# Performance work log

Hardware: AMD Instinct MI355X
Metric: run time of the kernel (lower is better)

The kernel has to match this reference:

```python
import jax, jax.numpy as jnp
import numpy as np

FILTERS = 128
KERNEL = 3
N_TAPS = KERNEL * KERNEL  # 9
STRIDES = 1


def setup_inputs() -> dict:
    key = jax.random.key(0)
    k1, k2, k3 = jax.random.split(key, 3)
    x = jax.random.normal(k1, (8, 128, 128, 64), dtype=jnp.float32)
    offsets = jax.random.normal(k2, (8, 128, 128, 2 * N_TAPS), dtype=jnp.float32)
    W = jax.random.normal(k3, (64, N_TAPS, FILTERS), dtype=jnp.float32) * 0.05
    return {"x": x, "offsets": offsets, "W": W}


def _blin(x, offsets, strides):
    # x: (m, Hi, Wi, C); offsets: (m, Ho, Wo, 2N) -> sampled (m, Ho, Wo, N, C)
    m, Hi, Wi, C = x.shape
    _, Ho, Wo, twoN = offsets.shape
    N = twoN // 2
    off = offsets.reshape(m, Ho, Wo, N, 2)
    base_i = jnp.arange(0, Hi, strides, dtype=jnp.float32)[:Ho]  # strided input rows
    base_j = jnp.arange(0, Wi, strides, dtype=jnp.float32)[:Wo]
    ci = jnp.clip(base_i[None, :, None, None] + off[..., 0], 0.0, Hi - 1.0)  # (m,Ho,Wo,N)
    cj = jnp.clip(base_j[None, None, :, None] + off[..., 1], 0.0, Wi - 1.0)
    i0 = jnp.floor(ci).astype(jnp.int32)
    i1 = jnp.ceil(ci).astype(jnp.int32)
    j0 = jnp.floor(cj).astype(jnp.int32)
    j1 = jnp.ceil(cj).astype(jnp.int32)
    fi = (ci - i0.astype(jnp.float32))[..., None]  # (m,Ho,Wo,N,1)
    fj = (cj - j0.astype(jnp.float32))[..., None]
    b = jnp.arange(m)[:, None, None, None]
    # four-corner gathers over channel vectors -> (m,Ho,Wo,N,C)
    v_lt = x[b, i0, j0]
    v_rt = x[b, i0, j1]
    v_lb = x[b, i1, j0]
    v_rb = x[b, i1, j1]
    v_t = v_lt + (v_rt - v_lt) * fj
    v_b = v_lb + (v_rb - v_lb) * fj
    return v_t + (v_b - v_t) * fi


def reference(x, offsets, W):
    sampled = _blin(x, offsets, STRIDES)  # (m,Ho,Wo,N,C)
    # sum over kernel taps N and channels C with W (C,N,filters)
    return jnp.einsum('mhwnc,cnf->mhwf', sampled, W)
```

## Files before the change

kernel.cpp:

```cpp
#include <hip/hip_runtime.h>
#include <hip/hip_fp16.h>
#include <cstddef>


typedef __attribute__((ext_vector_type(8))) _Float16 f16x8;
typedef __attribute__((ext_vector_type(4))) float    f32x4;

struct __align__(16) H2x4 { __half2 a, b, c, d; };


__global__ void cvt_x_kernel(const float* __restrict__ x, __half* __restrict__ xh) {
    int i = blockIdx.x * 256 + threadIdx.x;
    const float4* p = (const float4*)x + (size_t)i * 2;
    float4 a = p[0], b = p[1];
    H2x4 o;
    o.a = __floats2half2_rn(a.x, a.y);
    o.b = __floats2half2_rn(a.z, a.w);
    o.c = __floats2half2_rn(b.x, b.y);
    o.d = __floats2half2_rn(b.z, b.w);
    ((H2x4*)xh)[i] = o;
}

__global__ void cvt_w_kernel(const float* __restrict__ W, __half* __restrict__ wt2) {
    int idx = blockIdx.x * 256 + threadIdx.x;
    if (idx >= 9 * 4 * 4 * 64 * 8) return;
    int e  = idx & 7;
    int ln = (idx >> 3) & 63;
    int fr = (idx >> 9) & 3;
    int wv = (idx >> 11) & 3;
    int n  = idx >> 13;
    int nf = fr >> 1, kf = fr & 1;
    int r = ln & 15, g = ln >> 4;
    int c = kf * 32 + g * 8 + e;
    int f = wv * 32 + nf * 16 + r;
    wt2[idx] = __float2half_rn(W[((size_t)c * 9 + n) * 128 + f]);
}



struct Gather {
    H2x4 v00, v01, v10, v11;
    __half2 wA, wB;
};

__device__ inline void issue_gather(const char* __restrict__ ximg,
                                    const unsigned short* __restrict__ pb,
                                    const __half2 (*__restrict__ pw)[2],
                                    int px, int c8, Gather& G)
{
    int base = pb[px];
    G.wA = pw[px][0];
    G.wB = pw[px][1];
    int i0 = base >> 7, j0 = base & 127;
    size_t b00 = ((size_t)base << 7) + (c8 << 4);
    int di = (i0 < 127) ? (128 * 128) : 0;
    int dj = (j0 < 127) ? 128 : 0;
    G.v00 = *(const H2x4*)(ximg + b00);
    G.v01 = *(const H2x4*)(ximg + b00 + dj);
    G.v10 = *(const H2x4*)(ximg + b00 + di);
    G.v11 = *(const H2x4*)(ximg + b00 + di + dj);
}

__device__ inline void blend_store(char* __restrict__ buf, unsigned byteoff, const Gather& G)
{
    __half2 w00 = __low2half2(G.wA), w01 = __high2half2(G.wA);
    __half2 w10 = __low2half2(G.wB), w11 = __high2half2(G.wB);
    H2x4 r;
    r.a = __hfma2(G.v11.a, w11, __hfma2(G.v10.a, w10, __hfma2(G.v01.a, w01, __hmul2(G.v00.a, w00))));
    r.b = __hfma2(G.v11.b, w11, __hfma2(G.v10.b, w10, __hfma2(G.v01.b, w01, __hmul2(G.v00.b, w00))));
    r.c = __hfma2(G.v11.c, w11, __hfma2(G.v10.c, w10, __hfma2(G.v01.c, w01, __hmul2(G.v00.c, w00))));
    r.d = __hfma2(G.v11.d, w11, __hfma2(G.v10.d, w10, __hfma2(G.v01.d, w01, __hmul2(G.v00.d, w00))));
    *(H2x4*)(buf + byteoff) = r;
}

__device__ inline void lds_barrier() {
    __builtin_amdgcn_sched_barrier(0);
    asm volatile("s_waitcnt lgkmcnt(0)" ::: "memory");
    __builtin_amdgcn_s_barrier();
    __builtin_amdgcn_sched_barrier(0);
}

__global__ __launch_bounds__(256, 4)
void defconv_mfma(const float* __restrict__ offs,
                  const __half* __restrict__ xh,
                  const __half* __restrict__ wt,
                  float* __restrict__ out)
{
    __shared__ char sbuf[2][32 * 128];
    __shared__ unsigned short p_base[9][32];
    __shared__ __half2 p_w[9][32][2];

    const int t = threadIdx.x;

    int bid = blockIdx.x;
    int wid = (bid & 7) * 512 + (bid >> 3);
    const int m   = wid >> 9;
    const int h   = (wid >> 2) & 127;
    const int q   = wid & 3;
    const int pxg = q * 32;

    const float* offrow = offs + ((size_t)((m * 128 + h) * 128 + pxg)) * 18;
    for (int i = t; i < 288; i += 256) {
        int px = i & 31, n = i >> 5;
        float o0 = offrow[px * 18 + 2 * n];
        float o1 = offrow[px * 18 + 2 * n + 1];
        float ci = fminf(fmaxf((float)h + o0, 0.f), 127.f);
        float cj = fminf(fmaxf((float)(pxg + px) + o1, 0.f), 127.f);
        int i0 = (int)ci;
        int j0 = (int)cj;
        float fi = ci - (float)i0, fj = cj - (float)j0;
        float gi = 1.f - fi,       gj = 1.f - fj;
        p_base[n][px] = (unsigned short)((i0 << 7) | j0);
        p_w[n][px][0] = __floats2half2_rn(gi * gj, gi * fj);
        p_w[n][px][1] = __floats2half2_rn(fi * gj, fi * fj);
    }

    const char* ximg = (const char*)(xh + (size_t)m * (128 * 128 * 64));
    const int ln = t & 63;
    const int wv = t >> 6;
    const int r  = ln & 15;
    const int g  = ln >> 4;
    const int n0 = wv * 32;
    const unsigned rmask = (unsigned)((r & 7) << 4);

    const int px0 = t >> 3;
    const int c8  = t & 7;
    const unsigned off0 = (unsigned)(px0 * 128 + ((c8 * 16) ^ ((px0 & 7) << 4)));

    f32x4 acc[2][2] = {};

    __syncthreads();

    Gather G0;

    issue_gather(ximg, p_base[0], p_w[0], px0, c8, G0);
    blend_store(sbuf[0], off0, G0);
    issue_gather(ximg, p_base[1], p_w[1], px0, c8, G0);
    lds_barrier();

#pragma unroll 2
    for (int n = 0; n < 9; ++n) {
        char* cur = sbuf[n & 1];
        char* nxt = sbuf[(n + 1) & 1];

        f16x8 bfrag[2][2];
        const __half* wb = wt + (size_t)(n * 4 + wv) * (4 * 512);
#pragma unroll
        for (int nf = 0; nf < 2; ++nf)
#pragma unroll
            for (int kf = 0; kf < 2; ++kf)
                bfrag[nf][kf] = *(const f16x8*)(wb + ((nf * 2 + kf) * 64 + ln) * 8);

        if (n < 8) blend_store(nxt, off0, G0);
        if (n < 7) issue_gather(ximg, p_base[n + 2], p_w[n + 2], px0, c8, G0);

        __builtin_amdgcn_s_setprio(1);
#pragma unroll
        for (int mf = 0; mf < 2; ++mf) {
            int row = mf * 16 + r;
            unsigned o0 = (unsigned)(row * 128) + ((unsigned)(g * 16)      ^ rmask);
            unsigned o1 = (unsigned)(row * 128) + ((unsigned)(g * 16 + 64) ^ rmask);
            f16x8 a0 = *(const f16x8*)(cur + o0);
            f16x8 a1 = *(const f16x8*)(cur + o1);
            acc[mf][0] = __builtin_amdgcn_mfma_f32_16x16x32_f16(a0, bfrag[0][0], acc[mf][0], 0, 0, 0);
            acc[mf][1] = __builtin_amdgcn_mfma_f32_16x16x32_f16(a0, bfrag[1][0], acc[mf][1], 0, 0, 0);
            acc[mf][0] = __builtin_amdgcn_mfma_f32_16x16x32_f16(a1, bfrag[0][1], acc[mf][0], 0, 0, 0);
            acc[mf][1] = __builtin_amdgcn_mfma_f32_16x16x32_f16(a1, bfrag[1][1], acc[mf][1], 0, 0, 0);
        }
        __builtin_amdgcn_s_setprio(0);

        lds_barrier();
    }

    float* orow = out + ((size_t)((m * 128 + h) * 128 + pxg)) * 128;
#pragma unroll
    for (int mf = 0; mf < 2; ++mf)
#pragma unroll
        for (int nf = 0; nf < 2; ++nf) {
            int f    = n0 + nf * 16 + r;
            int px0e = mf * 16 + g * 4;
#pragma unroll
            for (int qq = 0; qq < 4; ++qq)
                orow[(size_t)(px0e + qq) * 128 + f] = acc[mf][nf][qq];
        }
}


constexpr int Hh   = 128;
constexpr int Wdim = 128;
constexpr int Cc   = 64;
constexpr int NTAP = 9;
constexpr int Ff   = 128;
constexpr int PXB  = 128;
constexpr int SPAD = 132;

__global__ __launch_bounds__(256, 2)
void defconv_f32(const float* __restrict__ x,
                 const float* __restrict__ offs,
                 const float* __restrict__ Wt,
                 float* __restrict__ out)
{
    __shared__ float s_tile[Cc][SPAD];
    __shared__ float w_tile[Cc][Ff];
    __shared__ float off_lds[PXB * 2 * NTAP];

    const int t   = threadIdx.x;
    const int bid = blockIdx.x;
    const int m   = bid >> 7;
    const int h   = bid & 127;

    const float* offrow = offs + (size_t)(m * Hh + h) * Wdim * (2 * NTAP);
    for (int i = t; i < PXB * 2 * NTAP; i += 256) off_lds[i] = offrow[i];

    const int pg = t & 15;
    const int fg = t >> 4;
    const int p0 = pg * 8;
    const int f0 = fg * 8;

    float acc[8][8];
#pragma unroll
    for (int a = 0; a < 8; ++a)
#pragma unroll
        for (int b = 0; b < 8; ++b) acc[a][b] = 0.f;

    const float* xbase = x + (size_t)m * Hh * Wdim * Cc;
    __syncthreads();

    for (int n = 0; n < NTAP; ++n) {
#pragma unroll
        for (int i = 0; i < 8; ++i) {
            int idx = t + 256 * i;
            int c   = idx >> 5;
            int f4  = (idx & 31) * 4;
            *(float4*)&w_tile[c][f4] =
                *(const float4*)(Wt + ((size_t)c * NTAP + n) * Ff + f4);
        }
#pragma unroll
        for (int i = 0; i < 8; ++i) {
            int task = t + 256 * i;
            int px   = task >> 4;
            int c4   = (task & 15) * 4;
            float o0 = off_lds[px * (2 * NTAP) + 2 * n];
            float o1 = off_lds[px * (2 * NTAP) + 2 * n + 1];
            float ci = fminf(fmaxf((float)h  + o0, 0.f), 127.f);
            float cj = fminf(fmaxf((float)px + o1, 0.f), 127.f);
            int i0 = (int)floorf(ci);
            int i1 = (int)ceilf(ci);
            int j0 = (int)floorf(cj);
            int j1 = (int)ceilf(cj);
            float fi = ci - (float)i0;
            float fj = cj - (float)j0;
            const float* r00 = xbase + ((size_t)i0 * Wdim + j0) * Cc + c4;
            const float* r01 = xbase + ((size_t)i0 * Wdim + j1) * Cc + c4;
            const float* r10 = xbase + ((size_t)i1 * Wdim + j0) * Cc + c4;
            const float* r11 = xbase + ((size_t)i1 * Wdim + j1) * Cc + c4;
            float4 vlt = *(const float4*)r00;
            float4 vrt = *(const float4*)r01;
            float4 vlb = *(const float4*)r10;
            float4 vrb = *(const float4*)r11;
            {
                float vt = vlt.x + (vrt.x - vlt.x) * fj;
                float vb = vlb.x + (vrb.x - vlb.x) * fj;
                s_tile[c4 + 0][px] = vt + (vb - vt) * fi;
            }
            {
                float vt = vlt.y + (vrt.y - vlt.y) * fj;
                float vb = vlb.y + (vrb.y - vlb.y) * fj;
                s_tile[c4 + 1][px] = vt + (vb - vt) * fi;
            }
            {
                float vt = vlt.z + (vrt.z - vlt.z) * fj;
                float vb = vlb.z + (vrb.z - vlb.z) * fj;
                s_tile[c4 + 2][px] = vt + (vb - vt) * fi;
            }
            {
                float vt = vlt.w + (vrt.w - vlt.w) * fj;
                float vb = vlb.w + (vrb.w - vlb.w) * fj;
                s_tile[c4 + 3][px] = vt + (vb - vt) * fi;
            }
        }
        __syncthreads();
        for (int c = 0; c < Cc; ++c) {
            float a[8], b[8];
            *(float4*)&a[0] = *(const float4*)&s_tile[c][p0];
            *(float4*)&a[4] = *(const float4*)&s_tile[c][p0 + 4];
            *(float4*)&b[0] = *(const float4*)&w_tile[c][f0];
            *(float4*)&b[4] = *(const float4*)&w_tile[c][f0 + 4];
#pragma unroll
            for (int pp = 0; pp < 8; ++pp)
#pragma unroll
                for (int ff = 0; ff < 8; ++ff)
                    acc[pp][ff] = fmaf(a[pp], b[ff], acc[pp][ff]);
        }
        __syncthreads();
    }

    float* orow = out + (size_t)(m * Hh + h) * Wdim * Ff;
#pragma unroll
    for (int pp = 0; pp < 8; ++pp) {
        float4 v0 = make_float4(acc[pp][0], acc[pp][1], acc[pp][2], acc[pp][3]);
        float4 v1 = make_float4(acc[pp][4], acc[pp][5], acc[pp][6], acc[pp][7]);
        *(float4*)&orow[(size_t)(p0 + pp) * Ff + f0]     = v0;
        *(float4*)&orow[(size_t)(p0 + pp) * Ff + f0 + 4] = v1;
    }
}


extern "C" void kernel_launch(void* const* d_in, const int* in_sizes, int n_in,
                              void* d_out, int out_size, void* d_ws, size_t ws_size,
                              hipStream_t stream) {
    const float* x    = (const float*)d_in[0];
    const float* offs = (const float*)d_in[1];
    const float* W    = (const float*)d_in[2];
    float* out        = (float*)d_out;

    const size_t XH_BYTES = (size_t)8 * 128 * 128 * 64 * 2;
    const size_t WT_BYTES = (size_t)9 * 4 * 4 * 64 * 8 * 2;

    if (ws_size >= XH_BYTES + WT_BYTES) {
        __half* xh = (__half*)d_ws;
        __half* wt = (__half*)((char*)d_ws + XH_BYTES);
        cvt_w_kernel<<<dim3(288),  dim3(256), 0, stream>>>(W, wt);
        cvt_x_kernel<<<dim3(4096), dim3(256), 0, stream>>>(x, xh);
        defconv_mfma<<<dim3(4096), dim3(256), 0, stream>>>(offs, xh, wt, out);
    } else {
        defconv_f32<<<dim3(1024), dim3(256), 0, stream>>>(x, offs, W, out);
    }
}
```

Before: 64.49 us.

## Double pixel tile to 64 per block with 8 waves each owning 16 filters

The MFMA kernel now processes 64 pixels per block with 512 threads. Each of the 8 waves computes a 16-filter slice over four 16-row M fragments instead of a 32-filter slice over two. The weight pre-layout is reorganized to match, so each wave loads only two B fragments per tap. This halves the number of blocks and reuses each weight fragment across more pixels, in exchange for larger LDS use per block and a different occupancy and gather balance.

```diff
diff --git a/kernel.cpp b/kernel.cpp
--- a/kernel.cpp
+++ b/kernel.cpp
@@ -21,19 +21,17 @@
     ((H2x4*)xh)[i] = o;
 }
 
-__global__ void cvt_w_kernel(const float* __restrict__ W, __half* __restrict__ wt2) {
+__global__ void cvt_w_kernel(const float* __restrict__ W, __half* __restrict__ wt8) {
     int idx = blockIdx.x * 256 + threadIdx.x;
-    if (idx >= 9 * 4 * 4 * 64 * 8) return;
+    if (idx >= 9 * 8 * 2 * 64 * 8) return;
     int e  = idx & 7;
     int ln = (idx >> 3) & 63;
-    int fr = (idx >> 9) & 3;
-    int wv = (idx >> 11) & 3;
+    int kf = (idx >> 9) & 1;
+    int wv = (idx >> 10) & 7;
     int n  = idx >> 13;
-    int nf = fr >> 1, kf = fr & 1;
-    int r = ln & 15, g = ln >> 4;
-    int c = kf * 32 + g * 8 + e;
-    int f = wv * 32 + nf * 16 + r;
-    wt2[idx] = __float2half_rn(W[((size_t)c * 9 + n) * 128 + f]);
+    int c = kf * 32 + (ln >> 4) * 8 + e;
+    int f = wv * 16 + (ln & 15);
+    wt8[idx] = __float2half_rn(W[((size_t)c * 9 + n) * 128 + f]);
 }
 
 
@@ -80,28 +78,28 @@
     __builtin_amdgcn_sched_barrier(0);
 }
 
-__global__ __launch_bounds__(256, 4)
+__global__ __launch_bounds__(512, 8)
 void defconv_mfma(const float* __restrict__ offs,
                   const __half* __restrict__ xh,
                   const __half* __restrict__ wt,
                   float* __restrict__ out)
 {
-    __shared__ char sbuf[2][32 * 128];
-    __shared__ unsigned short p_base[9][32];
-    __shared__ __half2 p_w[9][32][2];
+    __shared__ char sbuf[2][64 * 128];
+    __shared__ unsigned short p_base[9][64];
+    __shared__ __half2 p_w[9][64][2];
 
     const int t = threadIdx.x;
 
     int bid = blockIdx.x;
-    int wid = (bid & 7) * 512 + (bid >> 3);
-    const int m   = wid >> 9;
-    const int h   = (wid >> 2) & 127;
-    const int q   = wid & 3;
-    const int pxg = q * 32;
+    int wid = (bid & 7) * 256 + (bid >> 3);
+    const int m   = wid >> 8;
+    const int h   = (wid >> 1) & 127;
+    const int q   = wid & 1;
+    const int pxg = q * 64;
 
     const float* offrow = offs + ((size_t)((m * 128 + h) * 128 + pxg)) * 18;
-    for (int i = t; i < 288; i += 256) {
-        int px = i & 31, n = i >> 5;
+    for (int i = t; i < 576; i += 512) {
+        int px = i & 63, n = i >> 6;
         float o0 = offrow[px * 18 + 2 * n];
         float o1 = offrow[px * 18 + 2 * n + 1];
         float ci = fminf(fmaxf((float)h + o0, 0.f), 127.f);
@@ -120,14 +118,14 @@
     const int wv = t >> 6;
     const int r  = ln & 15;
     const int g  = ln >> 4;
-    const int n0 = wv * 32;
+    const int n0 = wv * 16;
     const unsigned rmask = (unsigned)((r & 7) << 4);
 
     const int px0 = t >> 3;
     const int c8  = t & 7;
     const unsigned off0 = (unsigned)(px0 * 128 + ((c8 * 16) ^ ((px0 & 7) << 4)));
 
-    f32x4 acc[2][2] = {};
+    f32x4 acc[4] = {};
 
     __syncthreads();
 
@@ -143,29 +141,25 @@
         char* cur = sbuf[n & 1];
         char* nxt = sbuf[(n + 1) & 1];
 
-        f16x8 bfrag[2][2];
-        const __half* wb = wt + (size_t)(n * 4 + wv) * (4 * 512);
-#pragma unroll
-        for (int nf = 0; nf < 2; ++nf)
-#pragma unroll
-            for (int kf = 0; kf < 2; ++kf)
-                bfrag[nf][kf] = *(const f16x8*)(wb + ((nf * 2 + kf) * 64 + ln) * 8);
+        f16x8 bfrag[2];
+        const __half* wb = wt + (size_t)(n * 8 + wv) * 1024;
+#pragma unroll
+        for (int kf = 0; kf < 2; ++kf)
+            bfrag[kf] = *(const f16x8*)(wb + (kf * 64 + ln) * 8);
 
         if (n < 8) blend_store(nxt, off0, G0);
         if (n < 7) issue_gather(ximg, p_base[n + 2], p_w[n + 2], px0, c8, G0);
 
         __builtin_amdgcn_s_setprio(1);
 #pragma unroll
-        for (int mf = 0; mf < 2; ++mf) {
+        for (int mf = 0; mf < 4; ++mf) {
             int row = mf * 16 + r;
             unsigned o0 = (unsigned)(row * 128) + ((unsigned)(g * 16)      ^ rmask);
             unsigned o1 = (unsigned)(row * 128) + ((unsigned)(g * 16 + 64) ^ rmask);
             f16x8 a0 = *(const f16x8*)(cur + o0);
             f16x8 a1 = *(const f16x8*)(cur + o1);
-            acc[mf][0] = __builtin_amdgcn_mfma_f32_16x16x32_f16(a0, bfrag[0][0], acc[mf][0], 0, 0, 0);
-            acc[mf][1] = __builtin_amdgcn_mfma_f32_16x16x32_f16(a0, bfrag[1][0], acc[mf][1], 0, 0, 0);
-            acc[mf][0] = __builtin_amdgcn_mfma_f32_16x16x32_f16(a1, bfrag[0][1], acc[mf][0], 0, 0, 0);
-            acc[mf][1] = __builtin_amdgcn_mfma_f32_16x16x32_f16(a1, bfrag[1][1], acc[mf][1], 0, 0, 0);
+            acc[mf] = __builtin_amdgcn_mfma_f32_16x16x32_f16(a0, bfrag[0], acc[mf], 0, 0, 0);
+            acc[mf] = __builtin_amdgcn_mfma_f32_16x16x32_f16(a1, bfrag[1], acc[mf], 0, 0, 0);
         }
         __builtin_amdgcn_s_setprio(0);
 
@@ -173,16 +167,14 @@
     }
 
     float* orow = out + ((size_t)((m * 128 + h) * 128 + pxg)) * 128;
-#pragma unroll
-    for (int mf = 0; mf < 2; ++mf)
-#pragma unroll
-        for (int nf = 0; nf < 2; ++nf) {
-            int f    = n0 + nf * 16 + r;
-            int px0e = mf * 16 + g * 4;
-#pragma unroll
-            for (int qq = 0; qq < 4; ++qq)
-                orow[(size_t)(px0e + qq) * 128 + f] = acc[mf][nf][qq];
-        }
+    const int f = n0 + r;
+#pragma unroll
+    for (int mf = 0; mf < 4; ++mf) {
+        int px0e = mf * 16 + g * 4;
+#pragma unroll
+        for (int qq = 0; qq < 4; ++qq)
+            orow[(size_t)(px0e + qq) * 128 + f] = acc[mf][qq];
+    }
 }
 
 
@@ -315,14 +307,14 @@
     float* out        = (float*)d_out;
 
     const size_t XH_BYTES = (size_t)8 * 128 * 128 * 64 * 2;
-    const size_t WT_BYTES = (size_t)9 * 4 * 4 * 64 * 8 * 2;
+    const size_t WT_BYTES = (size_t)9 * 8 * 2 * 64 * 8 * 2;
 
     if (ws_size >= XH_BYTES + WT_BYTES) {
         __half* xh = (__half*)d_ws;
         __half* wt = (__half*)((char*)d_ws + XH_BYTES);
         cvt_w_kernel<<<dim3(288),  dim3(256), 0, stream>>>(W, wt);
         cvt_x_kernel<<<dim3(4096), dim3(256), 0, stream>>>(x, xh);
-        defconv_mfma<<<dim3(4096), dim3(256), 0, stream>>>(offs, xh, wt, out);
+        defconv_mfma<<<dim3(2048), dim3(512), 0, stream>>>(offs, xh, wt, out);
     } else {
         defconv_f32<<<dim3(1024), dim3(256), 0, stream>>>(x, offs, W, out);
     }
```

After: 59.48 us. 1.08x faster.
